# Kernel tuning notes

Hardware: AMD Instinct MI355X
Metric: run time of the kernel (lower is better)

The kernel has to match this reference:

```python
import jax, jax.numpy as jnp
import numpy as np

N = 100_000      # nodes
E = 1_600_000    # edges (avg degree 16)
D_IN = 64        # node feature dim
H = 128          # hidden
E_IN = 64        # edge feature dim
C = 8            # num classes
EPS = 1e-5       # BatchNorm eps


def setup_inputs() -> dict:
    key = jax.random.key(0)
    ks = jax.random.split(key, 22)
    w = lambda k, shape: jax.random.normal(k, shape, dtype=jnp.float32) * 0.05
    return {
        "x_nodes": jax.random.normal(ks[0], (N, D_IN), dtype=jnp.float32),
        "e_feat": jax.random.normal(ks[1], (E, E_IN), dtype=jnp.float32),
        # SAGE layer 1 (fc_self, fc_neigh, bias)
        "Ws1": w(ks[2], (D_IN, H)), "Wn1": w(ks[3], (D_IN, H)), "b1": w(ks[4], (H,)),
        "g1": 1.0 + 0.1 * jax.random.normal(ks[5], (H,), dtype=jnp.float32),
        "bt1": 0.1 * jax.random.normal(ks[6], (H,), dtype=jnp.float32),
        # SAGE layer 2
        "Ws2": w(ks[7], (H, H)), "Wn2": w(ks[8], (H, H)), "b2": w(ks[9], (H,)),
        "g2": 1.0 + 0.1 * jax.random.normal(ks[10], (H,), dtype=jnp.float32),
        "bt2": 0.1 * jax.random.normal(ks[11], (H,), dtype=jnp.float32),
        # Edge MLP
        "We1": w(ks[12], (2 * H + E_IN, H)), "be1": w(ks[13], (H,)),
        "We2": w(ks[14], (H, C)), "be2": w(ks[15], (C,)),
        # Graph structure (message-flow graph, reused for both layers) and pair graph
        "src": jax.random.randint(ks[16], (E,), 0, N, dtype=jnp.int32),
        "dst": jax.random.randint(ks[17], (E,), 0, N, dtype=jnp.int32),
        "u": jax.random.randint(ks[18], (E,), 0, N, dtype=jnp.int32),
        "v": jax.random.randint(ks[19], (E,), 0, N, dtype=jnp.int32),
    }


def _sage_mean(h, src, dst, inv_deg, Ws, Wn, b):
    # DGL SAGEConv('mean'): rst = fc_self(h_dst) + fc_neigh(mean_{in-neighbors} h_src) + bias
    agg = jax.ops.segment_sum(h[src], dst, num_segments=h.shape[0]) * inv_deg[:, None]
    return h @ Ws + agg @ Wn + b


def _bn_relu(h, gamma, beta):
    # BatchNorm1d (training-mode batch stats, biased variance) + ReLU
    mu = h.mean(axis=0)
    var = jnp.mean((h - mu) ** 2, axis=0)
    return jax.nn.relu((h - mu) * jax.lax.rsqrt(var + EPS) * gamma + beta)


def reference(x_nodes, e_feat, Ws1, Wn1, b1, g1, bt1, Ws2, Wn2, b2, g2, bt2,
              We1, be1, We2, be2, src, dst, u, v):
    n = x_nodes.shape[0]
    deg = jax.ops.segment_sum(jnp.ones_like(src, dtype=x_nodes.dtype), dst, num_segments=n)
    inv_deg = jnp.where(deg > 0, 1.0 / jnp.maximum(deg, 1.0), 0.0)  # zero-degree -> 0 (DGL mean)
    h = _bn_relu(_sage_mean(x_nodes, src, dst, inv_deg, Ws1, Wn1, b1), g1, bt1)
    h = _bn_relu(_sage_mean(h, src, dst, inv_deg, Ws2, Wn2, b2), g2, bt2)
    # edge head: gather endpoints, concat with edge features, MLP (dropout = eval identity)
    e_repr = jnp.concatenate([h[u], h[v], e_feat], axis=1)  # [E, 2H + E_IN]
    hid = jax.nn.relu(e_repr @ We1 + be1)
    return hid @ We2 + be2
```

## Files before the change

kernel.cpp:

```cpp
#include <hip/hip_runtime.h>

#define NN 100000
#define EE 1600000
constexpr float BN_EPS = 1e-5f;

typedef __attribute__((ext_vector_type(8))) short short8;
typedef __attribute__((ext_vector_type(4))) float f32x4;

__device__ __forceinline__ short f2bf(float f) {
    unsigned u = __float_as_uint(f);
    u += 0x7fff + ((u >> 16) & 1);
    return (short)(u >> 16);
}
__device__ __forceinline__ float bf2f(short s) {
    return __uint_as_float(((unsigned)(unsigned short)s) << 16);
}

typedef __attribute__((address_space(1))) const unsigned int guint;
typedef __attribute__((address_space(3))) unsigned int luint;
__device__ __forceinline__ void gload_lds16(const void* g, void* l) {
    __builtin_amdgcn_global_load_lds((guint*)g, (luint*)l, 16, 0, 0);
}

__global__ void k_count(const int* __restrict__ dst, int* __restrict__ cnt) {
    int e = blockIdx.x * 256 + threadIdx.x;
    if (e < EE) atomicAdd(&cnt[dst[e]], 1);
}

__global__ __launch_bounds__(1024) void k_scan_part(const int* __restrict__ cnt,
                                                    int* __restrict__ bsum) {
    const int t = threadIdx.x, lane = t & 63, w = t >> 6;
    int i = blockIdx.x * 1024 + t;
    int v = (i < NN) ? cnt[i] : 0;
#pragma unroll
    for (int d = 1; d < 64; d <<= 1) v += __shfl_xor(v, d, 64);
    __shared__ int ws[16];
    if (lane == 0) ws[w] = v;
    __syncthreads();
    if (t == 0) {
        int s = 0;
#pragma unroll
        for (int k = 0; k < 16; ++k) s += ws[k];
        bsum[blockIdx.x] = s;
    }
}

__global__ void k_scan_base(int* __restrict__ bsum, int* __restrict__ offs, int nb) {
    if (threadIdx.x == 0) {
        int run = 0;
        for (int k = 0; k < nb; ++k) {
            int v = bsum[k];
            bsum[k] = run;
            run += v;
        }
        offs[NN] = run;
    }
}

__global__ __launch_bounds__(1024) void k_scan_final(const int* __restrict__ cnt,
                                                     const int* __restrict__ bsum,
                                                     int* __restrict__ offs,
                                                     int* __restrict__ cursor,
                                                     float* __restrict__ invd) {
    const int t = threadIdx.x, lane = t & 63, w = t >> 6;
    __shared__ int wsum[16], wexcl[16];
    int i = blockIdx.x * 1024 + t;
    int v = (i < NN) ? cnt[i] : 0;
    int s = v;
#pragma unroll
    for (int d = 1; d < 64; d <<= 1) {
        int o = __shfl_up(s, d, 64);
        if (lane >= d) s += o;
    }
    if (lane == 63) wsum[w] = s;
    __syncthreads();
    if (t < 16) {
        int wv = wsum[t];
        int ss = wv;
#pragma unroll
        for (int d = 1; d < 16; d <<= 1) {
            int o = __shfl_up(ss, d, 16);
            if (t >= d) ss += o;
        }
        wexcl[t] = ss - wv;
    }
    __syncthreads();
    if (i < NN) {
        int o = bsum[blockIdx.x] + (s - v) + wexcl[w];
        offs[i] = o;
        cursor[i] = o;
        invd[i] = v > 0 ? 1.f / (float)v : 0.f;
    }
}

__global__ void k_fill(const int* __restrict__ src, const int* __restrict__ dst,
                       int* __restrict__ cursor, int* __restrict__ eidsrc) {
    int e = blockIdx.x * 256 + threadIdx.x;
    if (e < EE) {
        int pos = atomicAdd(&cursor[dst[e]], 1);
        eidsrc[pos] = src[e];
    }
}

__global__ void k_f2bf(const float* __restrict__ in, short* __restrict__ out, int n8) {
    int i = blockIdx.x * 256 + threadIdx.x;
    if (i >= n8) return;
    float4 a = ((const float4*)in)[i * 2];
    float4 b = ((const float4*)in)[i * 2 + 1];
    short8 o;
    o[0] = f2bf(a.x); o[1] = f2bf(a.y); o[2] = f2bf(a.z); o[3] = f2bf(a.w);
    o[4] = f2bf(b.x); o[5] = f2bf(b.y); o[6] = f2bf(b.z); o[7] = f2bf(b.w);
    ((short8*)out)[i] = o;
}

template <int F>
__global__ __launch_bounds__(256) void k_gather_bf(
    const short* __restrict__ hbsrc, const int* __restrict__ offs,
    const int* __restrict__ eidsrc, const float* __restrict__ invd,
    short* __restrict__ aggb) {
    constexpr int G = F / 8;
    int gid = blockIdx.x * 256 + threadIdx.x;
    int node = gid / G;
    int sub = gid % G;
    if (node >= NN) return;
    int beg = offs[node], end = offs[node + 1];
    float iv = invd[node];
    float s[8] = {0.f, 0.f, 0.f, 0.f, 0.f, 0.f, 0.f, 0.f};
    const size_t co = (size_t)sub * 8;
    int p = beg;
    for (; p + 8 <= end; p += 8) {
        int idx[8];
#pragma unroll
        for (int q = 0; q < 8; ++q) idx[q] = eidsrc[p + q];
        short8 r[8];
#pragma unroll
        for (int q = 0; q < 8; ++q)
            r[q] = *(const short8*)(hbsrc + (size_t)idx[q] * F + co);
#pragma unroll
        for (int q = 0; q < 8; ++q)
#pragma unroll
            for (int j = 0; j < 8; ++j) s[j] += bf2f(r[q][j]);
    }
    for (; p + 4 <= end; p += 4) {
        int i0 = eidsrc[p], i1 = eidsrc[p + 1], i2 = eidsrc[p + 2], i3 = eidsrc[p + 3];
        short8 r0 = *(const short8*)(hbsrc + (size_t)i0 * F + co);
        short8 r1 = *(const short8*)(hbsrc + (size_t)i1 * F + co);
        short8 r2 = *(const short8*)(hbsrc + (size_t)i2 * F + co);
        short8 r3 = *(const short8*)(hbsrc + (size_t)i3 * F + co);
#pragma unroll
        for (int j = 0; j < 8; ++j)
            s[j] += (bf2f(r0[j]) + bf2f(r1[j])) + (bf2f(r2[j]) + bf2f(r3[j]));
    }
    for (; p < end; ++p) {
        short8 r = *(const short8*)(hbsrc + (size_t)eidsrc[p] * F + co);
#pragma unroll
        for (int j = 0; j < 8; ++j) s[j] += bf2f(r[j]);
    }
    short8 o;
#pragma unroll
    for (int j = 0; j < 8; ++j) o[j] = f2bf(s[j] * iv);
    *(short8*)(aggb + (size_t)node * F + co) = o;
}

__device__ __forceinline__ void packW(const float* W, short* Wp, int local, int kbase) {
    int k = local >> 7, col = local & 127;
    int gk = k + kbase;
    int kc = gk >> 5, kw = gk & 31, bp = kw >> 3, j = kw & 7;
    int cb = col >> 4, n = col & 15;
    Wp[kc * 4096 + (cb * 64 + bp * 16 + n) * 8 + j] = f2bf(W[k * 128 + col]);
}

__global__ void k_pack_all(const float* __restrict__ We1, const float* __restrict__ Ws1,
                           const float* __restrict__ Wn1, const float* __restrict__ Ws2,
                           const float* __restrict__ Wn2, const float* __restrict__ We2,
                           short* __restrict__ Wp_e, short* __restrict__ Wp1,
                           short* __restrict__ Wp2, short* __restrict__ Wp2e) {
    int idx = blockIdx.x * 256 + threadIdx.x;
    if (idx < 40960) {
        packW(We1, Wp_e, idx, 0);
    } else if (idx < 49152) {
        packW(Ws1, Wp1, idx - 40960, 0);
    } else if (idx < 57344) {
        packW(Wn1, Wp1, idx - 49152, 64);
    } else if (idx < 73728) {
        packW(Ws2, Wp2, idx - 57344, 0);
    } else if (idx < 90112) {
        packW(Wn2, Wp2, idx - 73728, 128);
    } else if (idx < 92160) {
        int local = idx - 90112;
        int k = local >> 4, n = local & 15;
        float val = (n < 8) ? We2[k * 8 + n] : 0.f;
        int kc2 = k >> 5, kl = k & 31, bp = kl >> 3, j = kl & 7;
        Wp2e[(kc2 * 64 + bp * 16 + n) * 8 + j] = f2bf(val);
    }
}

template <int KC1, int KC2>
__global__ __launch_bounds__(256) void k_node_mfma(
    const short* __restrict__ A1, const short* __restrict__ A2,
    const short* __restrict__ Wp, const float* __restrict__ bias,
    float* __restrict__ outf, float* __restrict__ stats) {
    __shared__ __align__(16) short sbuf[16384];
    __shared__ float bs[128];
    __shared__ float reds[4][128], redss[4][128];
    const int t = threadIdx.x;
    if (t < 128) bs[t] = bias[t];
    const int rowbase = blockIdx.x * 128;
    const int lane = t & 63, w = t >> 6;
    const int fo = (lane >> 4) * 16 + (lane & 15);

    auto NSTAGE = [&](int kc, short* Ad, short* Bd) {
        const short* src;
        int kst, kloc;
        if (kc < KC1) { src = A1; kst = KC1 * 32; kloc = kc * 32; }
        else          { src = A2; kst = KC2 * 32; kloc = (kc - KC1) * 32; }
#pragma unroll
        for (int p = 0; p < 2; ++p) {
            int s = t + p * 256;
            int b = (s >> 4) & 3;
            int row = rowbase + ((s >> 6) << 4) + (s & 15);
            gload_lds16(src + (size_t)row * kst + kloc + b * 8, Ad + s * 8);
            gload_lds16(Wp + (size_t)kc * 4096 + s * 8, Bd + s * 8);
        }
    };

    f32x4 acc[2][8];
#pragma unroll
    for (int i = 0; i < 2; ++i)
#pragma unroll
        for (int j = 0; j < 8; ++j) acc[i][j] = (f32x4){0.f, 0.f, 0.f, 0.f};

    constexpr int KC = KC1 + KC2;
    NSTAGE(0, sbuf, sbuf + 4096);
    __syncthreads();
    for (int kc = 0; kc < KC; ++kc) {
        const int cur = kc & 1;
        short* Ac = sbuf + (cur ? 8192 : 0);
        short* Bc = Ac + 4096;
        if (kc + 1 < KC) {
            short* An = sbuf + (cur ? 0 : 8192);
            NSTAGE(kc + 1, An, An + 4096);
        }
        short8 a0 = *(const short8*)(Ac + (2 * w * 64 + fo) * 8);
        short8 a1 = *(const short8*)(Ac + ((2 * w + 1) * 64 + fo) * 8);
#pragma unroll
        for (int cb = 0; cb < 8; ++cb) {
            short8 bfr = *(const short8*)(Bc + (cb * 64 + fo) * 8);
            acc[0][cb] = __builtin_amdgcn_mfma_f32_16x16x32_bf16(a0, bfr, acc[0][cb], 0, 0, 0);
            acc[1][cb] = __builtin_amdgcn_mfma_f32_16x16x32_bf16(a1, bfr, acc[1][cb], 0, 0, 0);
        }
        __syncthreads();
    }

    float cs[8], css[8];
#pragma unroll
    for (int cb = 0; cb < 8; ++cb) { cs[cb] = 0.f; css[cb] = 0.f; }
#pragma unroll
    for (int rb2 = 0; rb2 < 2; ++rb2) {
        int rloc = 32 * w + rb2 * 16 + ((lane >> 4) << 2);
#pragma unroll
        for (int cb = 0; cb < 8; ++cb) {
            int col = cb * 16 + (lane & 15);
            float bb = bs[col];
#pragma unroll
            for (int i = 0; i < 4; ++i) {
                int row = rowbase + rloc + i;
                if (row < NN) {
                    float v = acc[rb2][cb][i] + bb;
                    outf[(size_t)row * 128 + col] = v;
                    cs[cb] += v;
                    css[cb] += v * v;
                }
            }
        }
    }
#pragma unroll
    for (int cb = 0; cb < 8; ++cb) {
        cs[cb] += __shfl_xor(cs[cb], 16);
        cs[cb] += __shfl_xor(cs[cb], 32);
        css[cb] += __shfl_xor(css[cb], 16);
        css[cb] += __shfl_xor(css[cb], 32);
    }
    if (lane < 16) {
#pragma unroll
        for (int cb = 0; cb < 8; ++cb) {
            reds[w][cb * 16 + lane] = cs[cb];
            redss[w][cb * 16 + lane] = css[cb];
        }
    }
    __syncthreads();
    if (t < 128) {
        atomicAdd(&stats[t], reds[0][t] + reds[1][t] + reds[2][t] + reds[3][t]);
    } else {
        int c = t - 128;
        atomicAdd(&stats[128 + c], redss[0][c] + redss[1][c] + redss[2][c] + redss[3][c]);
    }
}

__global__ void k_bnrelu_bf16(const float* __restrict__ h, const float* __restrict__ stats,
                              const float* __restrict__ g, const float* __restrict__ bt,
                              short* __restrict__ hb) {
    __shared__ float a_sh[128], b_sh[128];
    const int t = threadIdx.x;
    if (t < 128) {
        float mu = stats[t] * (1.f / NN);
        float var = stats[128 + t] * (1.f / NN) - mu * mu;
        float a = g[t] * rsqrtf(var + BN_EPS);
        a_sh[t] = a;
        b_sh[t] = bt[t] - mu * a;
    }
    __syncthreads();
    int gid = blockIdx.x * 256 + t;
    if (gid >= NN * 16) return;
    int c0 = (gid & 15) * 8;
    float4 v0 = reinterpret_cast<const float4*>(h)[gid * 2];
    float4 v1 = reinterpret_cast<const float4*>(h)[gid * 2 + 1];
    short8 o;
    o[0] = f2bf(fmaxf(fmaf(a_sh[c0 + 0], v0.x, b_sh[c0 + 0]), 0.f));
    o[1] = f2bf(fmaxf(fmaf(a_sh[c0 + 1], v0.y, b_sh[c0 + 1]), 0.f));
    o[2] = f2bf(fmaxf(fmaf(a_sh[c0 + 2], v0.z, b_sh[c0 + 2]), 0.f));
    o[3] = f2bf(fmaxf(fmaf(a_sh[c0 + 3], v0.w, b_sh[c0 + 3]), 0.f));
    o[4] = f2bf(fmaxf(fmaf(a_sh[c0 + 4], v1.x, b_sh[c0 + 4]), 0.f));
    o[5] = f2bf(fmaxf(fmaf(a_sh[c0 + 5], v1.y, b_sh[c0 + 5]), 0.f));
    o[6] = f2bf(fmaxf(fmaf(a_sh[c0 + 6], v1.z, b_sh[c0 + 6]), 0.f));
    o[7] = f2bf(fmaxf(fmaf(a_sh[c0 + 7], v1.w, b_sh[c0 + 7]), 0.f));
    reinterpret_cast<short8*>(hb)[gid] = o;
}

__global__ __launch_bounds__(256) void k_edge_mfma(
    const short* __restrict__ hb, const float* __restrict__ ef,
    const short* __restrict__ Wp, const short* __restrict__ Wp2e,
    const float* __restrict__ be1, const float* __restrict__ be2,
    const int* __restrict__ uu, const int* __restrict__ vv,
    float* __restrict__ out) {
    __shared__ __align__(16) short smem[24576];
    __shared__ float be1s[128];
    __shared__ int suv[256];
    const int t = threadIdx.x;
    const int eb = blockIdx.x * 128;
    if (t < 128) {
        suv[t] = uu[eb + t];
        suv[128 + t] = vv[eb + t];
        be1s[t] = be1[t];
    }
    __syncthreads();

    const int lane = t & 63, w = t >> 6;
    const int fo = (lane >> 4) * 16 + (lane & 15);
    const int srow = t >> 1;
    const int sb0 = (t & 1) * 2;
    const int sslotbase = (srow >> 4) * 64 + (srow & 15);

    short8 b2f[4];
#pragma unroll
    for (int kc2 = 0; kc2 < 4; ++kc2)
        b2f[kc2] = *(const short8*)(Wp2e + (kc2 * 64 + fo) * 8);

    auto STAGE = [&](int kc, short* Ad, short* Bd) {
        if (kc < 8) {
#pragma unroll
            for (int p = 0; p < 2; ++p) {
                int s = t + p * 256;
                int b = (s >> 4) & 3;
                int row = ((s >> 6) << 4) + (s & 15);
                const short* gsrc =
                    hb + (size_t)suv[(kc >= 4) * 128 + row] * 128 + (kc & 3) * 32 + b * 8;
                gload_lds16(gsrc, Ad + s * 8);
            }
        } else {
            const float* er = ef + (size_t)(eb + srow) * 64 + (kc - 8) * 32;
#pragma unroll
            for (int p = 0; p < 2; ++p) {
                int b = sb0 + p;
                float4 f0 = *(const float4*)(er + b * 8);
                float4 f1 = *(const float4*)(er + b * 8 + 4);
                short8 v8;
                v8[0] = f2bf(f0.x); v8[1] = f2bf(f0.y);
                v8[2] = f2bf(f0.z); v8[3] = f2bf(f0.w);
                v8[4] = f2bf(f1.x); v8[5] = f2bf(f1.y);
                v8[6] = f2bf(f1.z); v8[7] = f2bf(f1.w);
                *(short8*)(Ad + (sslotbase + b * 16) * 8) = v8;
            }
        }
#pragma unroll
        for (int p = 0; p < 2; ++p) {
            int s = t + p * 256;
            gload_lds16(Wp + (size_t)kc * 4096 + s * 8, Bd + s * 8);
        }
    };

    f32x4 acc[2][8];
#pragma unroll
    for (int i = 0; i < 2; ++i)
#pragma unroll
        for (int j = 0; j < 8; ++j) acc[i][j] = (f32x4){0.f, 0.f, 0.f, 0.f};

    STAGE(0, smem, smem + 4096);
    STAGE(1, smem + 8192, smem + 8192 + 4096);
    for (int kc = 0; kc < 10; ++kc) {
        if (kc < 8)
            asm volatile("s_waitcnt vmcnt(4) lgkmcnt(0)" ::: "memory");
        else if (kc == 8)
            asm volatile("s_waitcnt vmcnt(2) lgkmcnt(0)" ::: "memory");
        else
            asm volatile("s_waitcnt vmcnt(0) lgkmcnt(0)" ::: "memory");
        __builtin_amdgcn_s_barrier();
        __builtin_amdgcn_sched_barrier(0);
        if (kc + 2 < 10) {
            short* An = smem + ((kc + 2) % 3) * 8192;
            STAGE(kc + 2, An, An + 4096);
        }
        short* Ac = smem + (kc % 3) * 8192;
        short* Bc = Ac + 4096;
        short8 afr0 = *(const short8*)(Ac + ((2 * w) * 64 + fo) * 8);
        short8 afr1 = *(const short8*)(Ac + ((2 * w + 1) * 64 + fo) * 8);
#pragma unroll
        for (int cb = 0; cb < 8; ++cb) {
            short8 bfr = *(const short8*)(Bc + (cb * 64 + fo) * 8);
            acc[0][cb] = __builtin_amdgcn_mfma_f32_16x16x32_bf16(afr0, bfr, acc[0][cb], 0, 0, 0);
            acc[1][cb] = __builtin_amdgcn_mfma_f32_16x16x32_bf16(afr1, bfr, acc[1][cb], 0, 0, 0);
        }
    }
    __syncthreads();

    short* Hid = smem;
#pragma unroll
    for (int rb2 = 0; rb2 < 2; ++rb2)
#pragma unroll
        for (int cb = 0; cb < 8; ++cb) {
            int col = cb * 16 + (lane & 15);
            int rbase = 32 * w + rb2 * 16 + ((lane >> 4) << 2);
            float bb = be1s[col];
#pragma unroll
            for (int i = 0; i < 4; ++i)
                Hid[(rbase + i) * 136 + col] = f2bf(fmaxf(acc[rb2][cb][i] + bb, 0.f));
        }
    __syncthreads();

#pragma unroll
    for (int rf = 0; rf < 2; ++rf) {
        f32x4 a2 = (f32x4){0.f, 0.f, 0.f, 0.f};
        const int rbl = 32 * w + 16 * rf + (lane & 15);
#pragma unroll
        for (int kc2 = 0; kc2 < 4; ++kc2) {
            short8 af = *(const short8*)(Hid + rbl * 136 + kc2 * 32 + 8 * (lane >> 4));
            a2 = __builtin_amdgcn_mfma_f32_16x16x32_bf16(af, b2f[kc2], a2, 0, 0, 0);
        }
        int col = lane & 15;
        if (col < 8) {
            int r0 = eb + 32 * w + 16 * rf + 4 * (lane >> 4);
            float bb = be2[col];
#pragma unroll
            for (int i = 0; i < 4; ++i)
                out[(size_t)(r0 + i) * 8 + col] = a2[i] + bb;
        }
    }
}

extern "C" void kernel_launch(void* const* d_in, const int* in_sizes, int n_in,
                              void* d_out, int out_size, void* d_ws, size_t ws_size,
                              hipStream_t stream) {
    const float* x   = (const float*)d_in[0];
    const float* ef  = (const float*)d_in[1];
    const float* Ws1 = (const float*)d_in[2];
    const float* Wn1 = (const float*)d_in[3];
    const float* b1  = (const float*)d_in[4];
    const float* g1  = (const float*)d_in[5];
    const float* bt1 = (const float*)d_in[6];
    const float* Ws2 = (const float*)d_in[7];
    const float* Wn2 = (const float*)d_in[8];
    const float* b2  = (const float*)d_in[9];
    const float* g2  = (const float*)d_in[10];
    const float* bt2 = (const float*)d_in[11];
    const float* We1 = (const float*)d_in[12];
    const float* be1 = (const float*)d_in[13];
    const float* We2 = (const float*)d_in[14];
    const float* be2 = (const float*)d_in[15];
    const int* src = (const int*)d_in[16];
    const int* dst = (const int*)d_in[17];
    const int* u   = (const int*)d_in[18];
    const int* v   = (const int*)d_in[19];
    float* out = (float*)d_out;

    char* p = (char*)d_ws;
    auto take = [&](size_t bytes) {
        char* r = p;
        p += (bytes + 255) & ~(size_t)255;
        return r;
    };
    int* cnt     = (int*)take(NN * 4);
    float* stats = (float*)take(512 * 4);
    float* invd  = (float*)take(NN * 4);
    int* offs    = (int*)take((NN + 1) * 4);
    int* cursor  = (int*)take(NN * 4);
    int* bsum    = (int*)take(128 * 4);
    int* eidsrc  = (int*)take((size_t)EE * 4);
    short* Wp_e  = (short*)take(320 * 128 * 2);
    short* Wp1   = (short*)take(128 * 128 * 2);
    short* Wp2   = (short*)take(256 * 128 * 2);
    short* Wp2e  = (short*)take(256 * 8 * 2);
    short* xb    = (short*)take((size_t)NN * 64 * 2);
    short* agg1b = (short*)take((size_t)NN * 64 * 2);
    short* h1b   = (short*)take((size_t)NN * 128 * 2);
    short* agg2b = (short*)take((size_t)NN * 128 * 2);
    take(65536);
    float* h1 = out;
    float* h2 = out;
    short* hb = xb;

    const int NB = (NN + 1023) / 1024;

    hipMemsetAsync(cnt, 0, ((char*)stats - (char*)cnt) + 512 * 4, stream);
    k_count<<<(EE + 255) / 256, 256, 0, stream>>>(dst, cnt);
    k_scan_part<<<NB, 1024, 0, stream>>>(cnt, bsum);
    k_scan_base<<<1, 64, 0, stream>>>(bsum, offs, NB);
    k_scan_final<<<NB, 1024, 0, stream>>>(cnt, bsum, offs, cursor, invd);
    k_fill<<<(EE + 255) / 256, 256, 0, stream>>>(src, dst, cursor, eidsrc);
    k_pack_all<<<360, 256, 0, stream>>>(We1, Ws1, Wn1, Ws2, Wn2, We2, Wp_e, Wp1, Wp2, Wp2e);
    k_f2bf<<<(NN * 8 + 255) / 256, 256, 0, stream>>>(x, xb, NN * 8);

    k_gather_bf<64><<<(NN * 8 + 255) / 256, 256, 0, stream>>>(xb, offs, eidsrc, invd, agg1b);
    k_node_mfma<2, 2><<<(NN + 127) / 128, 256, 0, stream>>>(xb, agg1b, Wp1, b1, h1, stats);
    k_bnrelu_bf16<<<(NN * 16 + 255) / 256, 256, 0, stream>>>(h1, stats, g1, bt1, h1b);

    k_gather_bf<128><<<(NN * 16 + 255) / 256, 256, 0, stream>>>(h1b, offs, eidsrc, invd, agg2b);
    k_node_mfma<4, 4><<<(NN + 127) / 128, 256, 0, stream>>>(h1b, agg2b, Wp2, b2, h2, stats + 256);
    k_bnrelu_bf16<<<(NN * 16 + 255) / 256, 256, 0, stream>>>(h2, stats + 256, g2, bt2, hb);

    k_edge_mfma<<<EE / 128, 256, 0, stream>>>(hb, ef, Wp_e, Wp2e, be1, be2, u, v, out);
}
```

Baseline: 647.3 us.

## Triple-buffer node GEMM loads and store pre-BN activations as bf16

The node MFMA kernel now uses a three-stage LDS ring with explicit vmcnt waits and one barrier per k-step, so loads run two stages ahead instead of one. The pre-BatchNorm activations are written as bf16 instead of fp32, which halves the intermediate write and the read in the BN+ReLU kernel. Stats are still accumulated in fp32 before rounding. The cost is more LDS per block, which may lower occupancy, and a small loss of precision in the normalized activations.

```diff
diff --git a/kernel.cpp b/kernel.cpp
--- a/kernel.cpp
+++ b/kernel.cpp
@@ -199,8 +199,8 @@
 __global__ __launch_bounds__(256) void k_node_mfma(
     const short* __restrict__ A1, const short* __restrict__ A2,
     const short* __restrict__ Wp, const float* __restrict__ bias,
-    float* __restrict__ outf, float* __restrict__ stats) {
-    __shared__ __align__(16) short sbuf[16384];
+    short* __restrict__ outz, float* __restrict__ stats) {
+    __shared__ __align__(16) short sbuf[24576];
     __shared__ float bs[128];
     __shared__ float reds[4][128], redss[4][128];
     const int t = threadIdx.x;
@@ -208,6 +208,7 @@
     const int rowbase = blockIdx.x * 128;
     const int lane = t & 63, w = t >> 6;
     const int fo = (lane >> 4) * 16 + (lane & 15);
+    __syncthreads();
 
     auto NSTAGE = [&](int kc, short* Ad, short* Bd) {
         const short* src;
@@ -232,15 +233,20 @@
 
     constexpr int KC = KC1 + KC2;
     NSTAGE(0, sbuf, sbuf + 4096);
-    __syncthreads();
+    NSTAGE(1, sbuf + 8192, sbuf + 8192 + 4096);
     for (int kc = 0; kc < KC; ++kc) {
-        const int cur = kc & 1;
-        short* Ac = sbuf + (cur ? 8192 : 0);
+        if (kc < KC - 1)
+            asm volatile("s_waitcnt vmcnt(4) lgkmcnt(0)" ::: "memory");
+        else
+            asm volatile("s_waitcnt vmcnt(0) lgkmcnt(0)" ::: "memory");
+        __builtin_amdgcn_s_barrier();
+        __builtin_amdgcn_sched_barrier(0);
+        if (kc + 2 < KC) {
+            short* An = sbuf + ((kc + 2) % 3) * 8192;
+            NSTAGE(kc + 2, An, An + 4096);
+        }
+        short* Ac = sbuf + (kc % 3) * 8192;
         short* Bc = Ac + 4096;
-        if (kc + 1 < KC) {
-            short* An = sbuf + (cur ? 0 : 8192);
-            NSTAGE(kc + 1, An, An + 4096);
-        }
         short8 a0 = *(const short8*)(Ac + (2 * w * 64 + fo) * 8);
         short8 a1 = *(const short8*)(Ac + ((2 * w + 1) * 64 + fo) * 8);
 #pragma unroll
@@ -249,8 +255,8 @@
             acc[0][cb] = __builtin_amdgcn_mfma_f32_16x16x32_bf16(a0, bfr, acc[0][cb], 0, 0, 0);
             acc[1][cb] = __builtin_amdgcn_mfma_f32_16x16x32_bf16(a1, bfr, acc[1][cb], 0, 0, 0);
         }
-        __syncthreads();
-    }
+    }
+    __syncthreads();
 
     float cs[8], css[8];
 #pragma unroll
@@ -267,7 +273,7 @@
                 int row = rowbase + rloc + i;
                 if (row < NN) {
                     float v = acc[rb2][cb][i] + bb;
-                    outf[(size_t)row * 128 + col] = v;
+                    outz[(size_t)row * 128 + col] = f2bf(v);
                     cs[cb] += v;
                     css[cb] += v * v;
                 }
@@ -297,7 +303,7 @@
     }
 }
 
-__global__ void k_bnrelu_bf16(const float* __restrict__ h, const float* __restrict__ stats,
+__global__ void k_bnrelu_bf16(const short* __restrict__ z, const float* __restrict__ stats,
                               const float* __restrict__ g, const float* __restrict__ bt,
                               short* __restrict__ hb) {
     __shared__ float a_sh[128], b_sh[128];
@@ -313,17 +319,11 @@
     int gid = blockIdx.x * 256 + t;
     if (gid >= NN * 16) return;
     int c0 = (gid & 15) * 8;
-    float4 v0 = reinterpret_cast<const float4*>(h)[gid * 2];
-    float4 v1 = reinterpret_cast<const float4*>(h)[gid * 2 + 1];
+    short8 zv = reinterpret_cast<const short8*>(z)[gid];
     short8 o;
-    o[0] = f2bf(fmaxf(fmaf(a_sh[c0 + 0], v0.x, b_sh[c0 + 0]), 0.f));
-    o[1] = f2bf(fmaxf(fmaf(a_sh[c0 + 1], v0.y, b_sh[c0 + 1]), 0.f));
-    o[2] = f2bf(fmaxf(fmaf(a_sh[c0 + 2], v0.z, b_sh[c0 + 2]), 0.f));
-    o[3] = f2bf(fmaxf(fmaf(a_sh[c0 + 3], v0.w, b_sh[c0 + 3]), 0.f));
-    o[4] = f2bf(fmaxf(fmaf(a_sh[c0 + 4], v1.x, b_sh[c0 + 4]), 0.f));
-    o[5] = f2bf(fmaxf(fmaf(a_sh[c0 + 5], v1.y, b_sh[c0 + 5]), 0.f));
-    o[6] = f2bf(fmaxf(fmaf(a_sh[c0 + 6], v1.z, b_sh[c0 + 6]), 0.f));
-    o[7] = f2bf(fmaxf(fmaf(a_sh[c0 + 7], v1.w, b_sh[c0 + 7]), 0.f));
+#pragma unroll
+    for (int j = 0; j < 8; ++j)
+        o[j] = f2bf(fmaxf(fmaf(a_sh[c0 + j], bf2f(zv[j]), b_sh[c0 + j]), 0.f));
     reinterpret_cast<short8*>(hb)[gid] = o;
 }
 
@@ -504,8 +504,7 @@
     short* h1b   = (short*)take((size_t)NN * 128 * 2);
     short* agg2b = (short*)take((size_t)NN * 128 * 2);
     take(65536);
-    float* h1 = out;
-    float* h2 = out;
+    short* zb = (short*)out;
     short* hb = xb;
 
     const int NB = (NN + 1023) / 1024;
@@ -520,12 +519,12 @@
     k_f2bf<<<(NN * 8 + 255) / 256, 256, 0, stream>>>(x, xb, NN * 8);
 
     k_gather_bf<64><<<(NN * 8 + 255) / 256, 256, 0, stream>>>(xb, offs, eidsrc, invd, agg1b);
-    k_node_mfma<2, 2><<<(NN + 127) / 128, 256, 0, stream>>>(xb, agg1b, Wp1, b1, h1, stats);
-    k_bnrelu_bf16<<<(NN * 16 + 255) / 256, 256, 0, stream>>>(h1, stats, g1, bt1, h1b);
+    k_node_mfma<2, 2><<<(NN + 127) / 128, 256, 0, stream>>>(xb, agg1b, Wp1, b1, zb, stats);
+    k_bnrelu_bf16<<<(NN * 16 + 255) / 256, 256, 0, stream>>>(zb, stats, g1, bt1, h1b);
 
     k_gather_bf<128><<<(NN * 16 + 255) / 256, 256, 0, stream>>>(h1b, offs, eidsrc, invd, agg2b);
-    k_node_mfma<4, 4><<<(NN + 127) / 128, 256, 0, stream>>>(h1b, agg2b, Wp2, b2, h2, stats + 256);
-    k_bnrelu_bf16<<<(NN * 16 + 255) / 256, 256, 0, stream>>>(h2, stats + 256, g2, bt2, hb);
+    k_node_mfma<4, 4><<<(NN + 127) / 128, 256, 0, stream>>>(h1b, agg2b, Wp2, b2, zb, stats + 256);
+    k_bnrelu_bf16<<<(NN * 16 + 255) / 256, 256, 0, stream>>>(zb, stats + 256, g2, bt2, hb);
 
     k_edge_mfma<<<EE / 128, 256, 0, stream>>>(hb, ef, Wp_e, Wp2e, be1, be2, u, v, out);
 }
```

Result: no change. 640.4 us (-1.1%).
